# Kernel optimization log

Measured on AMD Instinct MI355X. Metric: run time of the kernel, lower is better.

The kernel has to match this reference:

```python
import jax, jax.numpy as jnp
import numpy as np

B, R, S, C = 4, 16384, 96, 3

def setup_inputs() -> dict:
    key = jax.random.key(0)
    k1, k2, k3 = jax.random.split(key, 3)
    colors = jax.random.normal(k1, (B, R, S, C), dtype=jnp.float32)
    densities = jax.random.normal(k2, (B, R, S, 1), dtype=jnp.float32)
    # depths must be increasing along the sample axis (axis 2)
    depths = jnp.sort(
        jax.random.uniform(k3, (B, R, S, 1), dtype=jnp.float32, minval=2.0, maxval=6.0),
        axis=2,
    )
    return {"colors": colors, "densities": densities, "depths": depths}

def reference(colors, densities, depths):
    # clamp_mode == 'softplus', white_back == False (EG3D defaults)
    deltas = depths[:, :, 1:] - depths[:, :, :-1]                 # [B,R,S-1,1]
    colors_mid = (colors[:, :, :-1] + colors[:, :, 1:]) * 0.5     # [B,R,S-1,C]
    densities_mid = (densities[:, :, :-1] + densities[:, :, 1:]) * 0.5
    depths_mid = (depths[:, :, :-1] + depths[:, :, 1:]) * 0.5

    densities_mid = jax.nn.softplus(densities_mid - 1.0)
    density_delta = densities_mid * deltas
    alpha = 1.0 - jnp.exp(-density_delta)                         # [B,R,S-1,1]

    alpha_shifted = jnp.concatenate(
        [jnp.ones_like(alpha[:, :, :1]), 1.0 - alpha + 1e-10], axis=2
    )
    transmittance = jnp.cumprod(alpha_shifted, axis=2)[:, :, :-1]  # [B,R,S-1,1]
    weights = alpha * transmittance

    composite_rgb = jnp.sum(weights * colors_mid, axis=2)          # [B,R,C]
    weight_total = jnp.sum(weights, axis=2)                        # [B,R,1]
    composite_depth = jnp.sum(weights * depths_mid, axis=2) / weight_total
    composite_depth = jnp.nan_to_num(composite_depth, nan=jnp.inf)
    composite_depth = jnp.clip(composite_depth, jnp.min(depths), jnp.max(depths))

    composite_rgb = composite_rgb * 2.0 - 1.0
    return composite_rgb, composite_depth, weights
```

## Files before the change

### kernel.cpp

```cpp
#include <hip/hip_runtime.h>
#include <math.h>

#define NS 96
#define NSEG 95
#define LPR 16
#define SPL 6
#define RPB 16

__device__ __forceinline__ float fexp2(float x) { return __builtin_amdgcn_exp2f(x); }
__device__ __forceinline__ float flog2(float x) { return __builtin_amdgcn_logf(x); }

__device__ __forceinline__ void cp16(void* lds, const void* g) {
    __builtin_amdgcn_global_load_lds(
        (const __attribute__((address_space(1))) unsigned int*)g,
        (__attribute__((address_space(3))) unsigned int*)lds, 16, 0, 0);
}
__device__ __forceinline__ void cp4(void* lds, const void* g) {
    __builtin_amdgcn_global_load_lds(
        (const __attribute__((address_space(1))) unsigned int*)g,
        (__attribute__((address_space(3))) unsigned int*)lds, 4, 0, 0);
}

__device__ __forceinline__ float2 gl2(const float* p) {
    float2 r;
    asm volatile("global_load_dwordx2 %0, %1, off" : "=v"(r) : "v"(p));
    return r;
}
__device__ __forceinline__ float gl1(const float* p) {
    float r;
    asm volatile("global_load_dword %0, %1, off" : "=v"(r) : "v"(p));
    return r;
}

__global__ __launch_bounds__(256, 4) void raymarch_kernel(
    const float* __restrict__ colors,
    const float* __restrict__ densities,
    const float* __restrict__ depths,
    float* __restrict__ out_rgb,
    float* __restrict__ out_depth,
    float* __restrict__ out_w,
    int n_rays)
{
    __shared__ float scol[RPB * 288];

    const int tid  = threadIdx.x;
    const int wv   = tid >> 6;
    const int lane = tid & 63;
    const int sub  = tid & 15;
    const int rloc = tid >> 4;
    const int base = blockIdx.x * RPB;
    const int ray  = base + rloc;

    {
        const int wray = base + wv * 4;
        if (wray + 4 <= n_rays) {
            const float4* gq = (const float4*)colors + (size_t)wray * 72;
            float4* sq = (float4*)scol + wv * 288;
#pragma unroll
            for (int q = 0; q < 4; ++q)
                cp16(sq + 64 * q + lane, gq + 64 * q + lane);
            const float* gdw = colors + (size_t)wray * 288;
            float* sdw = scol + wv * 1152;
            cp4(sdw + 1024 + lane, gdw + 1024 + lane);
            cp4(sdw + 1088 + lane, gdw + 1088 + lane);
        }
    }

    if (ray >= n_rays) return;

    const int s0 = sub * SPL;
    const bool lastl = (sub == LPR - 1);

    const float* dep = depths    + (size_t)ray * NS + s0;
    const float* den = densities + (size_t)ray * NS + s0;

    float2 dv0 = gl2(dep + 0);
    float2 dv1 = gl2(dep + 2);
    float2 dv2 = gl2(dep + 4);
    float  d6  = gl1(dep + (lastl ? 5 : 6));
    float2 nv0 = gl2(den + 0);
    float2 nv1 = gl2(den + 2);
    float2 nv2 = gl2(den + 4);
    float  n6  = gl1(den + (lastl ? 5 : 6));

    asm volatile("s_waitcnt vmcnt(0)" ::: "memory");
    __builtin_amdgcn_sched_barrier(0);

    float d[7], nd[7];
    d[0] = dv0.x; d[1] = dv0.y; d[2] = dv1.x; d[3] = dv1.y;
    d[4] = dv2.x; d[5] = dv2.y; d[6] = d6;
    nd[0] = nv0.x; nd[1] = nv0.y; nd[2] = nv1.x; nd[3] = nv1.y;
    nd[4] = nv2.x; nd[5] = nv2.y; nd[6] = n6;

    const float LOG2E = 1.4426950408889634f;
    float e[SPL];
#pragma unroll
    for (int j = 0; j < SPL; ++j) {
        float delta = d[j + 1] - d[j];
        float x = (nd[j] + nd[j + 1]) * 0.5f - 1.0f;
        float sp2 = fmaxf(x, 0.f) * LOG2E + flog2(1.0f + fexp2(-fabsf(x) * LOG2E));
        e[j] = fexp2(-delta * sp2);
    }

    float P = 1.0f;
#pragma unroll
    for (int j = 0; j < SPL; ++j) P *= (e[j] + 1e-10f);
    float inc = P;
#pragma unroll
    for (int off = 1; off < LPR; off <<= 1) {
        float t = __shfl_up(inc, off, LPR);
        if (sub >= off) inc *= t;
    }
    float Tex = __shfl_up(inc, 1, LPR);
    if (sub == 0) Tex = 1.0f;

    float w[SPL];
    float sw = 0.f, sd = 0.f;
    {
        float T = Tex;
#pragma unroll
        for (int j = 0; j < SPL; ++j) {
            w[j] = (1.0f - e[j]) * T;
            T *= (e[j] + 1e-10f);
            sw += w[j];
            sd += w[j] * (d[j] + d[j + 1]);
        }
    }

    float rmax = __shfl(d[6], LPR - 1, LPR);
    float rmin = __shfl(d[0], 0, LPR);

    const float* lcol = scol + rloc * 288 + 3 * s0;
    float c[21];
#pragma unroll
    for (int q = 0; q < 9; ++q) {
        float2 v = *(const float2*)(lcol + 2 * q);
        c[2 * q] = v.x; c[2 * q + 1] = v.y;
    }
    {
        float2 v = *(const float2*)(lcol + (lastl ? 16 : 18));
        c[18] = v.x; c[19] = v.y;
        c[20] = lcol[lastl ? 17 : 20];
    }

    float sr = 0.f, sg = 0.f, sb = 0.f;
#pragma unroll
    for (int j = 0; j < SPL; ++j) {
        sr += w[j] * (c[3 * j + 0] + c[3 * j + 3]);
        sg += w[j] * (c[3 * j + 1] + c[3 * j + 4]);
        sb += w[j] * (c[3 * j + 2] + c[3 * j + 5]);
    }

#pragma unroll
    for (int off = 1; off < LPR; off <<= 1) {
        sw += __shfl_xor(sw, off, LPR);
        sd += __shfl_xor(sd, off, LPR);
        sr += __shfl_xor(sr, off, LPR);
        sg += __shfl_xor(sg, off, LPR);
        sb += __shfl_xor(sb, off, LPR);
    }

    float* wg = out_w + (size_t)ray * NSEG + s0;
    *(float2*)(wg + 0) = make_float2(w[0], w[1]);
    *(float2*)(wg + 2) = make_float2(w[2], w[3]);
    if (!lastl) {
        *(float2*)(wg + 4) = make_float2(w[4], w[5]);
    } else {
        wg[4] = w[4];
    }

    if (sub == 0) {
        float cd = (0.5f * sd) / sw;
        if (isnan(cd)) cd = __int_as_float(0x7F800000);
        cd = fminf(fmaxf(cd, rmin), rmax);
        out_depth[ray] = cd;
        out_rgb[(size_t)ray * 3 + 0] = sr - 1.0f;
        out_rgb[(size_t)ray * 3 + 1] = sg - 1.0f;
        out_rgb[(size_t)ray * 3 + 2] = sb - 1.0f;
    }
}

extern "C" void kernel_launch(void* const* d_in, const int* in_sizes, int n_in,
                              void* d_out, int out_size, void* d_ws, size_t ws_size,
                              hipStream_t stream) {
    const float* colors    = (const float*)d_in[0];
    const float* densities = (const float*)d_in[1];
    const float* depths    = (const float*)d_in[2];

    const int n_rays = in_sizes[1] / NS;

    float* out       = (float*)d_out;
    float* out_rgb   = out;
    float* out_depth = out + (size_t)n_rays * 3;
    float* out_w     = out + (size_t)n_rays * 4;

    hipLaunchKernelGGL(raymarch_kernel,
                       dim3((n_rays + RPB - 1) / RPB), dim3(256), 0, stream,
                       colors, densities, depths,
                       out_rgb, out_depth, out_w, n_rays);
}
```

Before: 27.02 us.

## Stage depths/densities via LDS async loads and coalesce weight stores through LDS

Depths and densities now come in through global_load_lds into shared memory with full-width coalesced 16-byte copies, in place of per-lane dwordx2 global loads. The weights output is written into the colors LDS buffer and then stored as contiguous float4 per wave instead of scattered float2 stores. A scalar fallback path covers partial waves. This adds LDS traffic and relies on wave-local ordering without an explicit LDS barrier between the weight write and the read-back, which could be a race.

```diff
diff --git a/kernel.cpp b/kernel.cpp
--- a/kernel.cpp
+++ b/kernel.cpp
@@ -19,17 +19,6 @@
     __builtin_amdgcn_global_load_lds(
         (const __attribute__((address_space(1))) unsigned int*)g,
         (__attribute__((address_space(3))) unsigned int*)lds, 4, 0, 0);
-}
-
-__device__ __forceinline__ float2 gl2(const float* p) {
-    float2 r;
-    asm volatile("global_load_dwordx2 %0, %1, off" : "=v"(r) : "v"(p));
-    return r;
-}
-__device__ __forceinline__ float gl1(const float* p) {
-    float r;
-    asm volatile("global_load_dword %0, %1, off" : "=v"(r) : "v"(p));
-    return r;
 }
 
 __global__ __launch_bounds__(256, 4) void raymarch_kernel(
@@ -42,55 +31,81 @@
     int n_rays)
 {
     __shared__ float scol[RPB * 288];
+    __shared__ float sdep[RPB * 96];
+    __shared__ float sden[RPB * 96];
 
     const int tid  = threadIdx.x;
     const int wv   = tid >> 6;
     const int lane = tid & 63;
     const int sub  = tid & 15;
-    const int rloc = tid >> 4;
+    const int g    = lane >> 4;
+    const int rloc = wv * 4 + g;
     const int base = blockIdx.x * RPB;
     const int ray  = base + rloc;
-
-    {
-        const int wray = base + wv * 4;
-        if (wray + 4 <= n_rays) {
-            const float4* gq = (const float4*)colors + (size_t)wray * 72;
-            float4* sq = (float4*)scol + wv * 288;
-#pragma unroll
-            for (int q = 0; q < 4; ++q)
-                cp16(sq + 64 * q + lane, gq + 64 * q + lane);
-            const float* gdw = colors + (size_t)wray * 288;
-            float* sdw = scol + wv * 1152;
-            cp4(sdw + 1024 + lane, gdw + 1024 + lane);
-            cp4(sdw + 1088 + lane, gdw + 1088 + lane);
+    const int wray = base + wv * 4;
+    const bool full = (wray + 4 <= n_rays);
+
+    if (full) {
+        const float4* gq = (const float4*)colors + (size_t)wray * 72;
+        float4* sq = (float4*)scol + wv * 288;
+#pragma unroll
+        for (int q = 0; q < 4; ++q)
+            cp16(sq + 64 * q + lane, gq + 64 * q + lane);
+        const float* gdw = colors + (size_t)wray * 288;
+        float* sdw = scol + wv * 1152;
+        cp4(sdw + 1024 + lane, gdw + 1024 + lane);
+        cp4(sdw + 1088 + lane, gdw + 1088 + lane);
+
+        const float4* gd = (const float4*)depths + (size_t)wray * 24;
+        float4* sd4 = (float4*)sdep + wv * 96;
+        cp16(sd4 + lane, gd + lane);
+        const float* gdd = depths + (size_t)wray * 96;
+        float* sdd = sdep + wv * 384;
+        cp4(sdd + 256 + lane, gdd + 256 + lane);
+        cp4(sdd + 320 + lane, gdd + 320 + lane);
+
+        const float4* gn = (const float4*)densities + (size_t)wray * 24;
+        float4* sn4 = (float4*)sden + wv * 96;
+        cp16(sn4 + lane, gn + lane);
+        const float* gnn = densities + (size_t)wray * 96;
+        float* snn = sden + wv * 384;
+        cp4(snn + 256 + lane, gnn + 256 + lane);
+        cp4(snn + 320 + lane, gnn + 320 + lane);
+    } else {
+        int r = wray + g;
+        if (r < n_rays) {
+            for (int t = sub; t < 288; t += 16)
+                scol[wv * 1152 + g * 288 + t] = colors[(size_t)r * 288 + t];
+            for (int t = sub; t < 96; t += 16) {
+                sdep[wv * 384 + g * 96 + t] = depths[(size_t)r * 96 + t];
+                sden[wv * 384 + g * 96 + t] = densities[(size_t)r * 96 + t];
+            }
         }
     }
+
+    asm volatile("s_waitcnt vmcnt(0)" ::: "memory");
+    __builtin_amdgcn_sched_barrier(0);
 
     if (ray >= n_rays) return;
 
     const int s0 = sub * SPL;
     const bool lastl = (sub == LPR - 1);
 
-    const float* dep = depths    + (size_t)ray * NS + s0;
-    const float* den = densities + (size_t)ray * NS + s0;
-
-    float2 dv0 = gl2(dep + 0);
-    float2 dv1 = gl2(dep + 2);
-    float2 dv2 = gl2(dep + 4);
-    float  d6  = gl1(dep + (lastl ? 5 : 6));
-    float2 nv0 = gl2(den + 0);
-    float2 nv1 = gl2(den + 2);
-    float2 nv2 = gl2(den + 4);
-    float  n6  = gl1(den + (lastl ? 5 : 6));
-
-    asm volatile("s_waitcnt vmcnt(0)" ::: "memory");
-    __builtin_amdgcn_sched_barrier(0);
+    const float* ldep = sdep + wv * 384 + g * 96 + s0;
+    const float* lden = sden + wv * 384 + g * 96 + s0;
 
     float d[7], nd[7];
-    d[0] = dv0.x; d[1] = dv0.y; d[2] = dv1.x; d[3] = dv1.y;
-    d[4] = dv2.x; d[5] = dv2.y; d[6] = d6;
-    nd[0] = nv0.x; nd[1] = nv0.y; nd[2] = nv1.x; nd[3] = nv1.y;
-    nd[4] = nv2.x; nd[5] = nv2.y; nd[6] = n6;
+    {
+        float2 v;
+        v = *(const float2*)(ldep + 0); d[0] = v.x; d[1] = v.y;
+        v = *(const float2*)(ldep + 2); d[2] = v.x; d[3] = v.y;
+        v = *(const float2*)(ldep + 4); d[4] = v.x; d[5] = v.y;
+        d[6] = ldep[lastl ? 5 : 6];
+        v = *(const float2*)(lden + 0); nd[0] = v.x; nd[1] = v.y;
+        v = *(const float2*)(lden + 2); nd[2] = v.x; nd[3] = v.y;
+        v = *(const float2*)(lden + 4); nd[4] = v.x; nd[5] = v.y;
+        nd[6] = lden[lastl ? 5 : 6];
+    }
 
     const float LOG2E = 1.4426950408889634f;
     float e[SPL];
@@ -127,10 +142,7 @@
         }
     }
 
-    float rmax = __shfl(d[6], LPR - 1, LPR);
-    float rmin = __shfl(d[0], 0, LPR);
-
-    const float* lcol = scol + rloc * 288 + 3 * s0;
+    const float* lcol = scol + wv * 1152 + g * 288 + 3 * s0;
     float c[21];
 #pragma unroll
     for (int q = 0; q < 9; ++q) {
@@ -160,16 +172,27 @@
         sb += __shfl_xor(sb, off, LPR);
     }
 
-    float* wg = out_w + (size_t)ray * NSEG + s0;
-    *(float2*)(wg + 0) = make_float2(w[0], w[1]);
-    *(float2*)(wg + 2) = make_float2(w[2], w[3]);
-    if (!lastl) {
-        *(float2*)(wg + 4) = make_float2(w[4], w[5]);
+    if (full) {
+        float* W = scol + wv * 1152;
+#pragma unroll
+        for (int j = 0; j < SPL; ++j)
+            if (!(lastl && j == SPL - 1)) W[g * NSEG + s0 + j] = w[j];
+        __builtin_amdgcn_sched_barrier(0);
+        const float4* W4 = (const float4*)W;
+        float4* go = (float4*)(out_w + (size_t)wray * NSEG);
+        go[lane] = W4[lane];
+        if (lane < 31) go[64 + lane] = W4[64 + lane];
     } else {
-        wg[4] = w[4];
+        float* wg = out_w + (size_t)ray * NSEG + s0;
+        *(float2*)(wg + 0) = make_float2(w[0], w[1]);
+        *(float2*)(wg + 2) = make_float2(w[2], w[3]);
+        if (!lastl) *(float2*)(wg + 4) = make_float2(w[4], w[5]);
+        else        wg[4] = w[4];
     }
 
     if (sub == 0) {
+        float rmin = sdep[wv * 384 + g * 96 + 0];
+        float rmax = sdep[wv * 384 + g * 96 + 95];
         float cd = (0.5f * sd) / sw;
         if (isnan(cd)) cd = __int_as_float(0x7F800000);
         cd = fminf(fmaxf(cd, rmin), rmax);
```

Result: slower. 27.87 us (+3.2%).
